# Performance work log

Measured on AMD Instinct MI355X. Metric: run time of the kernel, lower is better.

Reference implementation:

```python
import jax, jax.numpy as jnp
import numpy as np

N_NODES = 131072
D = 256            # nfeat_dim
E = 262144         # edges per graph (pos and neg)
IN_DIM = 2 * D     # 512
HID = IN_DIM // 2  # 256


def setup_inputs() -> dict:
    key = jax.random.key(0)
    k0, k1, k2, k3, k4, k5, k6 = jax.random.split(key, 7)
    block_outputs = jax.random.normal(k0, (N_NODES, D), dtype=jnp.float32)
    pos_src = jax.random.randint(k1, (E,), 0, N_NODES)
    pos_dst = jax.random.randint(k2, (E,), 0, N_NODES)
    neg_src = jax.random.randint(k3, (E,), 0, N_NODES)
    neg_dst = jax.random.randint(k4, (E,), 0, N_NODES)
    # LinkPredLayer params (xavier-normal-like init for weights)
    w1_std = float(np.sqrt(2.0 / (IN_DIM + HID)))
    w2_std = float(np.sqrt(2.0 / (HID + 1)))
    W1 = jax.random.normal(k5, (IN_DIM, HID), dtype=jnp.float32) * w1_std
    b1 = jnp.zeros((HID,), dtype=jnp.float32)
    W2 = jax.random.normal(k6, (HID, 1), dtype=jnp.float32) * w2_std
    b2 = jnp.zeros((1,), dtype=jnp.float32)
    return {"block_outputs": block_outputs, "pos_src": pos_src, "pos_dst": pos_dst,
            "neg_src": neg_src, "neg_dst": neg_dst,
            "W1": W1, "b1": b1, "W2": W2, "b2": b2}


def _linkpred_mlp(h, W1, b1, W2, b2):
    # eval mode: dropout = identity; BatchNorm defined in __init__ but unused in forward
    h = jax.nn.relu(h @ W1 + b1)        # [E_total, HID]
    return jax.nn.sigmoid(h @ W2 + b2)  # [E_total, 1]


def reference(block_outputs, pos_src, pos_dst, neg_src, neg_dst, W1, b1, W2, b2):
    # edge gather: src || dst concat per edge (apply_edges(linkpred_concat))
    pos_emb = jnp.concatenate([block_outputs[pos_src], block_outputs[pos_dst]], axis=1)  # [E, 2D]
    neg_emb = jnp.concatenate([block_outputs[neg_src], block_outputs[neg_dst]], axis=1)  # [E, 2D]
    emb = jnp.concatenate([pos_emb, neg_emb], axis=0)  # [2E, 2D]
    logits = _linkpred_mlp(emb, W1, b1, W2, b2)        # [2E, 1]
    labels = jnp.zeros_like(logits).at[:pos_emb.shape[0]].set(1.0)
    return logits.squeeze(-1), labels.squeeze(-1)
```

## Files before the change

### kernel.cpp

```cpp
#include <hip/hip_runtime.h>
#include <hip/hip_bf16.h>
#include <stdint.h>

#define E_EDGES 262144
#define DFEAT 256
#define KDIM 512
#define NNODES 131072

typedef __attribute__((ext_vector_type(8))) short short8;
typedef __attribute__((ext_vector_type(4))) float f32x4;

static __device__ __forceinline__ unsigned f2bf(float x) {
    unsigned u = __float_as_uint(x);
    u += 0x7fffu + ((u >> 16) & 1u);
    return u >> 16;
}
static __device__ __forceinline__ float bf2f(unsigned short s) {
    return __uint_as_float(((unsigned)s) << 16);
}

__global__ __launch_bounds__(256) void prep_wB2_kernel(const float* __restrict__ W1,
                                                       unsigned short* __restrict__ wB2) {
    int idx = blockIdx.x * 256 + threadIdx.x;
    int n = idx >> 8;
    int k = idx & 255;
    int srow = k + ((n >= 256) ? 256 : 0);
    wB2[((size_t)(k >> 3) * 512 + n) * 8 + (k & 7)] = (unsigned short)f2bf(W1[srow * 256 + (n & 255)]);
}

__global__ __launch_bounds__(512, 2) void gemm_uv5_kernel(const float* __restrict__ table,
                                                          const unsigned short* __restrict__ wB2,
                                                          unsigned short* __restrict__ uv) {
    __shared__ __align__(16) unsigned char lds[65536];

    const int tid = threadIdx.x;
    const int l = tid & 63;
    const int wv = tid >> 6;
    const int l15 = l & 15;
    const int lq = l >> 4;

    short8 bfr[8][4];
#pragma unroll
    for (int kk = 0; kk < 8; ++kk)
#pragma unroll
        for (int j = 0; j < 4; ++j) {
            int col = wv * 64 + j * 16 + l15;
            bfr[kk][j] = *(const short8*)(wB2 + ((size_t)(kk * 4 + lq) * 512 + col) * 8);
        }

    const int srow = tid >> 4;
    const int gc0 = (tid & 15) * 2;
    const int tile0 = blockIdx.x * 16;

    float4 sreg[4];
    auto loadA = [&](int t) {
        const float* src = table + (size_t)(tile0 + t) * 32 * DFEAT + (size_t)srow * DFEAT;
#pragma unroll
        for (int m = 0; m < 2; ++m) {
            sreg[m * 2]     = *(const float4*)(src + (gc0 + m) * 8);
            sreg[m * 2 + 1] = *(const float4*)(src + (gc0 + m) * 8 + 4);
        }
    };
    auto writeA = [&](int buf) {
        unsigned char* base = lds + buf * 16384 + srow * 512;
#pragma unroll
        for (int m = 0; m < 2; ++m) {
            int gc = gc0 + m;
            uint4 w;
            w.x = f2bf(sreg[m * 2].x)     | (f2bf(sreg[m * 2].y) << 16);
            w.y = f2bf(sreg[m * 2].z)     | (f2bf(sreg[m * 2].w) << 16);
            w.z = f2bf(sreg[m * 2 + 1].x) | (f2bf(sreg[m * 2 + 1].y) << 16);
            w.w = f2bf(sreg[m * 2 + 1].z) | (f2bf(sreg[m * 2 + 1].w) << 16);
            int phys = (gc & 16) | ((gc ^ (srow & 15)) & 15);
            *(uint4*)(base + phys * 16) = w;
        }
    };

    loadA(0);
    writeA(0);
    asm volatile("s_waitcnt lgkmcnt(0)" ::: "memory");
    __builtin_amdgcn_s_barrier();

    for (int t = 0; t < 16; ++t) {
        const int m0 = (tile0 + t) * 32;

        if (t < 15) loadA(t + 1);

        f32x4 acc[2][4];
#pragma unroll
        for (int i = 0; i < 2; ++i)
#pragma unroll
            for (int j = 0; j < 4; ++j)
                acc[i][j] = (f32x4){0.f, 0.f, 0.f, 0.f};

        const unsigned char* Ab = lds + (t & 1) * 16384;
#pragma unroll
        for (int kk = 0; kk < 8; ++kk) {
            int g = kk * 4 + lq;
            int phys = (g & 16) | ((g ^ l15) & 15);
            short8 af[2];
#pragma unroll
            for (int i = 0; i < 2; ++i)
                af[i] = *(const short8*)(Ab + (i * 16 + l15) * 512 + phys * 16);
#pragma unroll
            for (int i = 0; i < 2; ++i)
#pragma unroll
                for (int j = 0; j < 4; ++j)
                    acc[i][j] = __builtin_amdgcn_mfma_f32_16x16x32_bf16(bfr[kk][j], af[i], acc[i][j], 0, 0, 0);
        }

        unsigned char* Bnc = lds + 32768;
#pragma unroll
        for (int i = 0; i < 2; ++i)
#pragma unroll
            for (int j = 0; j < 4; ++j) {
                unsigned lo = f2bf(acc[i][j][0]) | (f2bf(acc[i][j][1]) << 16);
                unsigned hi = f2bf(acc[i][j][2]) | (f2bf(acc[i][j][3]) << 16);
                int nodep = i * 16 + l15;
                int colbyte = wv * 128 + j * 32 + lq * 8;
                int g = colbyte >> 4;
                int phys = (g & ~15) | ((g ^ nodep) & 15);
                *(uint2*)(Bnc + nodep * 1024 + phys * 16 + (colbyte & 15)) = make_uint2(lo, hi);
            }

        asm volatile("s_waitcnt lgkmcnt(0)" ::: "memory");
        __builtin_amdgcn_s_barrier();

#pragma unroll
        for (int p = 0; p < 4; ++p) {
            int node = p * 8 + (tid >> 6);
            int col16 = tid & 63;
            int phys = (col16 & ~15) | ((col16 ^ node) & 15);
            uint4 w = *(const uint4*)(Bnc + node * 1024 + phys * 16);
            *(uint4*)(uv + ((size_t)(m0 + node)) * 512 + col16 * 8) = w;
        }

        if (t < 15) writeA((t + 1) & 1);

        asm volatile("s_waitcnt lgkmcnt(0)" ::: "memory");
        __builtin_amdgcn_s_barrier();
    }
}

__global__ __launch_bounds__(256) void edge2_kernel(
    const unsigned short* __restrict__ uv,
    const int* __restrict__ pos_src, const int* __restrict__ pos_dst,
    const int* __restrict__ neg_src, const int* __restrict__ neg_dst,
    const float* __restrict__ b1, const float* __restrict__ W2,
    const float* __restrict__ b2,
    float* __restrict__ out) {

    const int tid = threadIdx.x;
    const int m = tid & 31;
    const int hw = tid >> 5;
    const int eb = blockIdx.x * 64;
    const int e0 = eb + hw * 8;
    const bool is_pos = (eb < E_EDGES);
    const int ee0 = is_pos ? e0 : e0 - E_EDGES;
    const int* __restrict__ srcp = is_pos ? pos_src : neg_src;
    const int* __restrict__ dstp = is_pos ? pos_dst : neg_dst;

    int4 sa = *(const int4*)(srcp + ee0);
    int4 sb = *(const int4*)(srcp + ee0 + 4);
    int4 da = *(const int4*)(dstp + ee0);
    int4 db = *(const int4*)(dstp + ee0 + 4);
    const int sidx[8] = {sa.x, sa.y, sa.z, sa.w, sb.x, sb.y, sb.z, sb.w};
    const int didx[8] = {da.x, da.y, da.z, da.w, db.x, db.y, db.z, db.w};

    short8 uvec[8], vvec[8];
#pragma unroll
    for (int j = 0; j < 8; ++j) {
        uvec[j] = *(const short8*)(uv + (size_t)sidx[j] * 512 + m * 8);
        vvec[j] = *(const short8*)(uv + (size_t)didx[j] * 512 + 256 + m * 8);
    }

    float b1a[8], w2a[8];
    *(float4*)&b1a[0] = *(const float4*)(b1 + m * 8);
    *(float4*)&b1a[4] = *(const float4*)(b1 + m * 8 + 4);
    *(float4*)&w2a[0] = *(const float4*)(W2 + m * 8);
    *(float4*)&w2a[4] = *(const float4*)(W2 + m * 8 + 4);
    const float b2v = b2[0];

    float p[8];
#pragma unroll
    for (int j = 0; j < 8; ++j) {
        float pp = 0.f;
#pragma unroll
        for (int i = 0; i < 8; ++i) {
            float z = bf2f((unsigned short)uvec[j][i]) + bf2f((unsigned short)vvec[j][i]) + b1a[i];
            z = fmaxf(z, 0.f);
            pp = fmaf(z, w2a[i], pp);
        }
#pragma unroll
        for (int mk = 1; mk < 32; mk <<= 1) pp += __shfl_xor(pp, mk, 64);
        p[j] = pp;
    }

    float pj = p[0];
#pragma unroll
    for (int k = 1; k < 8; ++k) if (m == k) pj = p[k];
    if (m < 8) {
        float x = pj + b2v;
        out[(size_t)e0 + m] = 1.0f / (1.0f + __expf(-x));
    }
    if (tid < 64)
        out[(size_t)(2 * E_EDGES) + eb + tid] = is_pos ? 1.0f : 0.0f;
}

__global__ __launch_bounds__(256) void conv_table_kernel(const float* __restrict__ t,
                                                         unsigned short* __restrict__ o) {
    int idx = blockIdx.x * 256 + threadIdx.x;
    float4 a = ((const float4*)t)[idx * 2];
    float4 b = ((const float4*)t)[idx * 2 + 1];
    uint4 w;
    w.x = f2bf(a.x) | (f2bf(a.y) << 16);
    w.y = f2bf(a.z) | (f2bf(a.w) << 16);
    w.z = f2bf(b.x) | (f2bf(b.y) << 16);
    w.w = f2bf(b.z) | (f2bf(b.w) << 16);
    ((uint4*)o)[idx] = w;
}

__global__ __launch_bounds__(256) void prep_w1t_kernel(const float* __restrict__ W1,
                                                       unsigned short* __restrict__ w1t) {
    int idx = blockIdx.x * 256 + threadIdx.x;
    int k = idx >> 8;
    int n = idx & 255;
    w1t[n * KDIM + k] = (unsigned short)f2bf(W1[idx]);
}

__global__ __launch_bounds__(256) void linkpred4_kernel(
    const unsigned short* __restrict__ tblb,
    const int* __restrict__ pos_src, const int* __restrict__ pos_dst,
    const int* __restrict__ neg_src, const int* __restrict__ neg_dst,
    const float* __restrict__ b1, const float* __restrict__ W2,
    const float* __restrict__ b2,
    const unsigned short* __restrict__ w1t,
    float* __restrict__ out) {

    __shared__ __align__(16) unsigned short Bs[64 * 512];

    const int tid = threadIdx.x;
    const int l = tid & 63;
    const int wv = tid >> 6;
    const int l15 = l & 15;
    const int lq = l >> 4;
    const int m0 = blockIdx.x * 128;
    const bool is_pos = (m0 < E_EDGES);

    int nsrc[2], ndst[2];
#pragma unroll
    for (int mt = 0; mt < 2; ++mt) {
        int m = m0 + wv * 32 + mt * 16 + l15;
        if (is_pos) { nsrc[mt] = pos_src[m];            ndst[mt] = pos_dst[m]; }
        else        { int mm = m - E_EDGES; nsrc[mt] = neg_src[mm]; ndst[mt] = neg_dst[mm]; }
    }

    auto stageB = [&](int c) {
#pragma unroll
        for (int i = 0; i < 16; ++i) {
            int lc = wv * 16 + i;
            int gc = c * 64 + lc;
            const unsigned short* g = w1t + (size_t)gc * KDIM + ((l ^ i) << 3);
            char* lp = (char*)Bs + lc * 1024;
            __builtin_amdgcn_global_load_lds(
                (const __attribute__((address_space(1))) void*)g,
                (__attribute__((address_space(3))) void*)lp, 16, 0, 0);
        }
    };

    stageB(0);
    __builtin_amdgcn_sched_barrier(0);

    short8 af[2][16];
#pragma unroll
    for (int h = 0; h < 16; ++h)
#pragma unroll
        for (int mt = 0; mt < 2; ++mt) {
            int node = (h < 8) ? nsrc[mt] : ndst[mt];
            const unsigned short* g = tblb + (size_t)node * DFEAT + (h & 7) * 32 + lq * 8;
            af[mt][h] = *(const short8*)g;
        }
    __builtin_amdgcn_sched_barrier(0);

    f32x4 acc[2][4];
#pragma unroll
    for (int mt = 0; mt < 2; ++mt)
#pragma unroll
        for (int j = 0; j < 4; ++j)
            acc[mt][j] = (f32x4){0.f, 0.f, 0.f, 0.f};
    float rowacc[2][4] = {{0.f, 0.f, 0.f, 0.f}, {0.f, 0.f, 0.f, 0.f}};

    const char* Bb = (const char*)Bs;

#pragma unroll
    for (int c = 0; c < 4; ++c) {
        if (c == 0) {
            asm volatile("s_waitcnt vmcnt(32)" ::: "memory");
        } else {
            __syncthreads();
            stageB(c);
#pragma unroll
            for (int mt = 0; mt < 2; ++mt)
#pragma unroll
                for (int j = 0; j < 4; ++j) {
                    int col = (c - 1) * 64 + j * 16 + l15;
                    float b1v = b1[col], w2v = W2[col];
#pragma unroll
                    for (int r = 0; r < 4; ++r) {
                        float hv = fmaxf(acc[mt][j][r] + b1v, 0.f);
                        rowacc[mt][r] = fmaf(hv, w2v, rowacc[mt][r]);
                    }
                    acc[mt][j] = (f32x4){0.f, 0.f, 0.f, 0.f};
                }
            asm volatile("s_waitcnt vmcnt(0)" ::: "memory");
        }
        __builtin_amdgcn_s_barrier();

        __builtin_amdgcn_s_setprio(1);
#pragma unroll
        for (int h = 0; h < 16; ++h) {
            short8 bf[4];
#pragma unroll
            for (int j = 0; j < 4; ++j) {
                int cl = j * 16 + l15;
                int phys = (h * 4 + lq) ^ l15;
                bf[j] = *(const short8*)(Bb + cl * 1024 + phys * 16);
            }
#pragma unroll
            for (int mt = 0; mt < 2; ++mt)
#pragma unroll
                for (int j = 0; j < 4; ++j)
                    acc[mt][j] = __builtin_amdgcn_mfma_f32_16x16x32_bf16(af[mt][h], bf[j], acc[mt][j], 0, 0, 0);
        }
        __builtin_amdgcn_s_setprio(0);
    }

#pragma unroll
    for (int mt = 0; mt < 2; ++mt)
#pragma unroll
        for (int j = 0; j < 4; ++j) {
            int col = 3 * 64 + j * 16 + l15;
            float b1v = b1[col], w2v = W2[col];
#pragma unroll
            for (int r = 0; r < 4; ++r) {
                float hv = fmaxf(acc[mt][j][r] + b1v, 0.f);
                rowacc[mt][r] = fmaf(hv, w2v, rowacc[mt][r]);
            }
        }

    const float b2v = b2[0];
#pragma unroll
    for (int mt = 0; mt < 2; ++mt)
#pragma unroll
        for (int r = 0; r < 4; ++r) {
            float p = rowacc[mt][r];
#pragma unroll
            for (int mk = 1; mk < 16; mk <<= 1) p += __shfl_xor(p, mk, 64);
            if (l15 == 0) {
                int m = m0 + wv * 32 + mt * 16 + lq * 4 + r;
                float sg = 1.0f / (1.0f + __expf(-(p + b2v)));
                out[(size_t)m] = sg;
                out[(size_t)(2 * E_EDGES) + m] = is_pos ? 1.0f : 0.0f;
            }
        }
}

__global__ __launch_bounds__(256) void linkpred_fb_kernel(
    const float* __restrict__ table,
    const int* __restrict__ pos_src, const int* __restrict__ pos_dst,
    const int* __restrict__ neg_src, const int* __restrict__ neg_dst,
    const float* __restrict__ b1, const float* __restrict__ W2,
    const float* __restrict__ b2,
    const unsigned short* __restrict__ w1t,
    float* __restrict__ out) {

    __shared__ __align__(16) unsigned short As[2][64 * 64];
    __shared__ int sIdx[64], dIdx[64];
    __shared__ float wpart[4][64];

    const int tid = threadIdx.x;
    const int l = tid & 63;
    const int wv = tid >> 6;
    const int m0 = blockIdx.x * 64;

    if (tid < 64) {
        int m = m0 + tid;
        int si, di;
        if (m < E_EDGES) { si = pos_src[m];            di = pos_dst[m]; }
        else             { si = neg_src[m - E_EDGES];  di = neg_dst[m - E_EDGES]; }
        sIdx[tid] = si;
        dIdx[tid] = di;
    }

    float b1v[4], w2v[4];
#pragma unroll
    for (int j = 0; j < 4; j++) {
        int n = wv * 64 + j * 16 + (l & 15);
        b1v[j] = b1[n];
        w2v[j] = W2[n];
    }

    __syncthreads();

    const int e0 = tid >> 3;
    const int q  = tid & 7;
    const int e1 = e0 + 32;

    auto pack_write = [&](int buf, int e, const float4& x, const float4& y) {
        uint4 w;
        w.x = f2bf(x.x) | (f2bf(x.y) << 16);
        w.y = f2bf(x.z) | (f2bf(x.w) << 16);
        w.z = f2bf(y.x) | (f2bf(y.y) << 16);
        w.w = f2bf(y.z) | (f2bf(y.w) << 16);
        int byte = e * 128 + q * 16;
        byte ^= (e & 7) << 4;
        *(uint4*)((char*)(&As[buf][0]) + byte) = w;
    };

    {
        const float* p0 = table + (size_t)sIdx[e0] * DFEAT + q * 8;
        const float* p1 = table + (size_t)sIdx[e1] * DFEAT + q * 8;
        float4 a0 = *(const float4*)p0, a1 = *(const float4*)(p0 + 4);
        float4 c0 = *(const float4*)p1, c1 = *(const float4*)(p1 + 4);
        pack_write(0, e0, a0, a1);
        pack_write(0, e1, c0, c1);
    }
    __syncthreads();

    f32x4 acc[4][4];
#pragma unroll
    for (int i = 0; i < 4; i++)
#pragma unroll
        for (int j = 0; j < 4; j++)
            acc[i][j] = (f32x4){0.f, 0.f, 0.f, 0.f};

    for (int s = 0; s < 8; s++) {
        float4 a0, a1, c0, c1;
        if (s < 7) {
            int sn = s + 1;
            const int* idxA = (sn < 4) ? sIdx : dIdx;
            int cb = (sn & 3) * 64 + q * 8;
            const float* p0 = table + (size_t)idxA[e0] * DFEAT + cb;
            const float* p1 = table + (size_t)idxA[e1] * DFEAT + cb;
            a0 = *(const float4*)p0; a1 = *(const float4*)(p0 + 4);
            c0 = *(const float4*)p1; c1 = *(const float4*)(p1 + 4);
        }

        const int cur = s & 1;
        const char* Abase = (const char*)(&As[cur][0]);
#pragma unroll
        for (int h = 0; h < 2; h++) {
            short8 af[4], bf[4];
#pragma unroll
            for (int i = 0; i < 4; i++) {
                int row = i * 16 + (l & 15);
                int byte = row * 128 + h * 64 + ((l >> 4) << 4);
                byte ^= (l & 7) << 4;
                af[i] = *(const short8*)(Abase + byte);
            }
#pragma unroll
            for (int j = 0; j < 4; j++) {
                int col = wv * 64 + j * 16 + (l & 15);
                int koff = s * 64 + h * 32 + ((l >> 4) << 3);
                bf[j] = *(const short8*)(w1t + col * KDIM + koff);
            }
#pragma unroll
            for (int i = 0; i < 4; i++)
#pragma unroll
                for (int j = 0; j < 4; j++)
                    acc[i][j] = __builtin_amdgcn_mfma_f32_16x16x32_bf16(af[i], bf[j], acc[i][j], 0, 0, 0);
        }

        if (s < 7) {
            pack_write((s + 1) & 1, e0, a0, a1);
            pack_write((s + 1) & 1, e1, c0, c1);
        }
        __syncthreads();
    }

    float part[16];
#pragma unroll
    for (int i = 0; i < 4; i++) {
#pragma unroll
        for (int r = 0; r < 4; r++) {
            float p = 0.f;
#pragma unroll
            for (int j = 0; j < 4; j++) {
                float hv = acc[i][j][r] + b1v[j];
                hv = fmaxf(hv, 0.f);
                p = fmaf(hv, w2v[j], p);
            }
#pragma unroll
            for (int mk = 1; mk < 16; mk <<= 1) p += __shfl_xor(p, mk, 64);
            part[i * 4 + r] = p;
        }
    }
    if ((l & 15) == 0) {
        int g = l >> 4;
#pragma unroll
        for (int i = 0; i < 4; i++)
#pragma unroll
            for (int r = 0; r < 4; r++)
                wpart[wv][i * 16 + g * 4 + r] = part[i * 4 + r];
    }
    __syncthreads();

    if (tid < 64) {
        float x = wpart[0][tid] + wpart[1][tid] + wpart[2][tid] + wpart[3][tid] + b2[0];
        float sg = 1.0f / (1.0f + __expf(-x));
        out[(size_t)m0 + tid] = sg;
        out[(size_t)(2 * E_EDGES) + m0 + tid] = (m0 < E_EDGES) ? 1.0f : 0.0f;
    }
}

extern "C" void kernel_launch(void* const* d_in, const int* in_sizes, int n_in,
                              void* d_out, int out_size, void* d_ws, size_t ws_size,
                              hipStream_t stream) {
    const float* table = (const float*)d_in[0];
    const int* ps = (const int*)d_in[1];
    const int* pd = (const int*)d_in[2];
    const int* ns = (const int*)d_in[3];
    const int* nd = (const int*)d_in[4];
    const float* W1 = (const float*)d_in[5];
    const float* b1 = (const float*)d_in[6];
    const float* W2 = (const float*)d_in[7];
    const float* b2 = (const float*)d_in[8];
    float* out = (float*)d_out;

    const size_t wB_bytes  = (size_t)KDIM * 256 * 2;
    const size_t uv_bytes  = (size_t)NNODES * KDIM * 2;
    const size_t tbl_bytes = (size_t)NNODES * DFEAT * 2;
    const size_t w1t_bytes = (size_t)256 * KDIM * 2;

    if (ws_size >= wB_bytes + uv_bytes) {
        unsigned short* wB2 = (unsigned short*)d_ws;
        unsigned short* uv = (unsigned short*)((char*)d_ws + wB_bytes);
        hipLaunchKernelGGL(prep_wB2_kernel, dim3(512), dim3(256), 0, stream, W1, wB2);
        hipLaunchKernelGGL(gemm_uv5_kernel, dim3(256), dim3(512), 0, stream, table, wB2, uv);
        hipLaunchKernelGGL(edge2_kernel, dim3(8192), dim3(256), 0, stream,
                           uv, ps, pd, ns, nd, b1, W2, b2, out);
    } else if (ws_size >= tbl_bytes + w1t_bytes) {
        unsigned short* tblb = (unsigned short*)d_ws;
        unsigned short* w1t = (unsigned short*)((char*)d_ws + tbl_bytes);
        hipLaunchKernelGGL(conv_table_kernel, dim3(16384), dim3(256), 0, stream, table, tblb);
        hipLaunchKernelGGL(prep_w1t_kernel, dim3(512), dim3(256), 0, stream, W1, w1t);
        hipLaunchKernelGGL(linkpred4_kernel, dim3(4096), dim3(256), 0, stream,
                           tblb, ps, pd, ns, nd, b1, W2, b2, w1t, out);
    } else {
        unsigned short* w1t = (unsigned short*)d_ws;
        hipLaunchKernelGGL(prep_w1t_kernel, dim3(512), dim3(256), 0, stream, W1, w1t);
        hipLaunchKernelGGL(linkpred_fb_kernel, dim3(8192), dim3(256), 0, stream,
                           table, ps, pd, ns, nd, b1, W2, b2, w1t, out);
    }
}
```

Before: 141.6 us.

## Deepen GEMM prefetch to two tiles and defer uv stores to next tile

The node-projection GEMM now holds two register buffers, so global loads for tile t+2 are issued while tile t computes, instead of only one tile ahead. The global store of each tile's bf16 result is moved into the start of the next iteration, after the barrier, so it overlaps with the next tile's MFMA work rather than sitting between barriers. The loop is manually unrolled by two through macros so the register buffers alternate. This raises register pressure and could reduce occupancy or cause spills under the (512,2) launch bounds.

```diff
diff --git a/kernel.cpp b/kernel.cpp
--- a/kernel.cpp
+++ b/kernel.cpp
@@ -28,7 +28,7 @@
     wB2[((size_t)(k >> 3) * 512 + n) * 8 + (k & 7)] = (unsigned short)f2bf(W1[srow * 256 + (n & 255)]);
 }
 
-__global__ __launch_bounds__(512, 2) void gemm_uv5_kernel(const float* __restrict__ table,
+__global__ __launch_bounds__(512, 2) void gemm_uv6_kernel(const float* __restrict__ table,
                                                           const unsigned short* __restrict__ wB2,
                                                           unsigned short* __restrict__ uv) {
     __shared__ __align__(16) unsigned char lds[65536];
@@ -52,94 +52,112 @@
     const int gc0 = (tid & 15) * 2;
     const int tile0 = blockIdx.x * 16;
 
-    float4 sreg[4];
-    auto loadA = [&](int t) {
-        const float* src = table + (size_t)(tile0 + t) * 32 * DFEAT + (size_t)srow * DFEAT;
-#pragma unroll
-        for (int m = 0; m < 2; ++m) {
-            sreg[m * 2]     = *(const float4*)(src + (gc0 + m) * 8);
-            sreg[m * 2 + 1] = *(const float4*)(src + (gc0 + m) * 8 + 4);
-        }
-    };
-    auto writeA = [&](int buf) {
-        unsigned char* base = lds + buf * 16384 + srow * 512;
-#pragma unroll
-        for (int m = 0; m < 2; ++m) {
-            int gc = gc0 + m;
-            uint4 w;
-            w.x = f2bf(sreg[m * 2].x)     | (f2bf(sreg[m * 2].y) << 16);
-            w.y = f2bf(sreg[m * 2].z)     | (f2bf(sreg[m * 2].w) << 16);
-            w.z = f2bf(sreg[m * 2 + 1].x) | (f2bf(sreg[m * 2 + 1].y) << 16);
-            w.w = f2bf(sreg[m * 2 + 1].z) | (f2bf(sreg[m * 2 + 1].w) << 16);
-            int phys = (gc & 16) | ((gc ^ (srow & 15)) & 15);
-            *(uint4*)(base + phys * 16) = w;
-        }
-    };
-
-    loadA(0);
-    writeA(0);
+    float4 sregA[4], sregB[4];
+
+#define LOADTO(T, S)                                                               \
+    {                                                                              \
+        const float* _src = table + (size_t)(tile0 + (T)) * 32 * DFEAT             \
+                            + (size_t)srow * DFEAT;                                \
+        _Pragma("unroll")                                                          \
+        for (int _m = 0; _m < 2; ++_m) {                                           \
+            S[_m * 2]     = *(const float4*)(_src + (gc0 + _m) * 8);               \
+            S[_m * 2 + 1] = *(const float4*)(_src + (gc0 + _m) * 8 + 4);           \
+        }                                                                          \
+    }
+
+#define WRITEA(BUF, S)                                                             \
+    {                                                                              \
+        unsigned char* _base = lds + (BUF) * 16384 + srow * 512;                   \
+        _Pragma("unroll")                                                          \
+        for (int _m = 0; _m < 2; ++_m) {                                           \
+            int _gc = gc0 + _m;                                                    \
+            uint4 _w;                                                              \
+            _w.x = f2bf(S[_m * 2].x)     | (f2bf(S[_m * 2].y) << 16);              \
+            _w.y = f2bf(S[_m * 2].z)     | (f2bf(S[_m * 2].w) << 16);              \
+            _w.z = f2bf(S[_m * 2 + 1].x) | (f2bf(S[_m * 2 + 1].y) << 16);          \
+            _w.w = f2bf(S[_m * 2 + 1].z) | (f2bf(S[_m * 2 + 1].w) << 16);          \
+            int _phys = (_gc & 16) | ((_gc ^ (srow & 15)) & 15);                   \
+            *(uint4*)(_base + _phys * 16) = _w;                                    \
+        }                                                                          \
+    }
+
+#define STORE_PREV(T)                                                              \
+    {                                                                              \
+        const int _m0 = (tile0 + (T)-1) * 32;                                      \
+        unsigned char* _bnc = lds + 32768;                                         \
+        _Pragma("unroll")                                                          \
+        for (int _p = 0; _p < 4; ++_p) {                                           \
+            int _node = _p * 8 + wv;                                               \
+            int _c16 = l;                                                          \
+            int _phys = (_c16 & ~15) | ((_c16 ^ _node) & 15);                      \
+            uint4 _w = *(const uint4*)(_bnc + _node * 1024 + _phys * 16);          \
+            *(uint4*)(uv + ((size_t)(_m0 + _node)) * 512 + _c16 * 8) = _w;         \
+        }                                                                          \
+    }
+
+#define TILE_BODY(T, LDST, WSRC, ABUF)                                             \
+    {                                                                              \
+        if ((T) > 0) STORE_PREV(T);                                                \
+        if ((T) + 2 < 16) LOADTO((T) + 2, LDST);                                   \
+        f32x4 acc[2][4];                                                           \
+        _Pragma("unroll")                                                          \
+        for (int _i = 0; _i < 2; ++_i)                                             \
+            _Pragma("unroll")                                                      \
+            for (int _j = 0; _j < 4; ++_j)                                         \
+                acc[_i][_j] = (f32x4){0.f, 0.f, 0.f, 0.f};                         \
+        const unsigned char* _Ab = lds + (ABUF) * 16384;                           \
+        _Pragma("unroll")                                                          \
+        for (int _kk = 0; _kk < 8; ++_kk) {                                        \
+            int _g = _kk * 4 + lq;                                                 \
+            int _phys = (_g & 16) | ((_g ^ l15) & 15);                             \
+            short8 _af[2];                                                         \
+            _Pragma("unroll")                                                      \
+            for (int _i = 0; _i < 2; ++_i)                                         \
+                _af[_i] = *(const short8*)(_Ab + (_i * 16 + l15) * 512 + _phys * 16); \
+            _Pragma("unroll")                                                      \
+            for (int _i = 0; _i < 2; ++_i)                                         \
+                _Pragma("unroll")                                                  \
+                for (int _j = 0; _j < 4; ++_j)                                     \
+                    acc[_i][_j] = __builtin_amdgcn_mfma_f32_16x16x32_bf16(         \
+                        bfr[_kk][_j], _af[_i], acc[_i][_j], 0, 0, 0);              \
+        }                                                                          \
+        asm volatile("s_waitcnt lgkmcnt(0)" ::: "memory");                         \
+        __builtin_amdgcn_s_barrier();                                              \
+        unsigned char* _bnc = lds + 32768;                                         \
+        _Pragma("unroll")                                                          \
+        for (int _i = 0; _i < 2; ++_i)                                             \
+            _Pragma("unroll")                                                      \
+            for (int _j = 0; _j < 4; ++_j) {                                       \
+                unsigned _lo = f2bf(acc[_i][_j][0]) | (f2bf(acc[_i][_j][1]) << 16);\
+                unsigned _hi = f2bf(acc[_i][_j][2]) | (f2bf(acc[_i][_j][3]) << 16);\
+                int _nodep = _i * 16 + l15;                                        \
+                int _cb = wv * 128 + _j * 32 + lq * 8;                             \
+                int _g = _cb >> 4;                                                 \
+                int _phys = (_g & ~15) | ((_g ^ _nodep) & 15);                     \
+                *(uint2*)(_bnc + _nodep * 1024 + _phys * 16 + (_cb & 15)) =        \
+                    make_uint2(_lo, _hi);                                          \
+            }                                                                      \
+        if ((T) < 15) WRITEA(((T) + 1) & 1, WSRC);                                 \
+        asm volatile("s_waitcnt lgkmcnt(0)" ::: "memory");                         \
+        __builtin_amdgcn_s_barrier();                                              \
+    }
+
+    LOADTO(0, sregA);
+    WRITEA(0, sregA);
+    LOADTO(1, sregB);
     asm volatile("s_waitcnt lgkmcnt(0)" ::: "memory");
     __builtin_amdgcn_s_barrier();
 
-    for (int t = 0; t < 16; ++t) {
-        const int m0 = (tile0 + t) * 32;
-
-        if (t < 15) loadA(t + 1);
-
-        f32x4 acc[2][4];
-#pragma unroll
-        for (int i = 0; i < 2; ++i)
-#pragma unroll
-            for (int j = 0; j < 4; ++j)
-                acc[i][j] = (f32x4){0.f, 0.f, 0.f, 0.f};
-
-        const unsigned char* Ab = lds + (t & 1) * 16384;
-#pragma unroll
-        for (int kk = 0; kk < 8; ++kk) {
-            int g = kk * 4 + lq;
-            int phys = (g & 16) | ((g ^ l15) & 15);
-            short8 af[2];
-#pragma unroll
-            for (int i = 0; i < 2; ++i)
-                af[i] = *(const short8*)(Ab + (i * 16 + l15) * 512 + phys * 16);
-#pragma unroll
-            for (int i = 0; i < 2; ++i)
-#pragma unroll
-                for (int j = 0; j < 4; ++j)
-                    acc[i][j] = __builtin_amdgcn_mfma_f32_16x16x32_bf16(bfr[kk][j], af[i], acc[i][j], 0, 0, 0);
-        }
-
-        unsigned char* Bnc = lds + 32768;
-#pragma unroll
-        for (int i = 0; i < 2; ++i)
-#pragma unroll
-            for (int j = 0; j < 4; ++j) {
-                unsigned lo = f2bf(acc[i][j][0]) | (f2bf(acc[i][j][1]) << 16);
-                unsigned hi = f2bf(acc[i][j][2]) | (f2bf(acc[i][j][3]) << 16);
-                int nodep = i * 16 + l15;
-                int colbyte = wv * 128 + j * 32 + lq * 8;
-                int g = colbyte >> 4;
-                int phys = (g & ~15) | ((g ^ nodep) & 15);
-                *(uint2*)(Bnc + nodep * 1024 + phys * 16 + (colbyte & 15)) = make_uint2(lo, hi);
-            }
-
-        asm volatile("s_waitcnt lgkmcnt(0)" ::: "memory");
-        __builtin_amdgcn_s_barrier();
-
-#pragma unroll
-        for (int p = 0; p < 4; ++p) {
-            int node = p * 8 + (tid >> 6);
-            int col16 = tid & 63;
-            int phys = (col16 & ~15) | ((col16 ^ node) & 15);
-            uint4 w = *(const uint4*)(Bnc + node * 1024 + phys * 16);
-            *(uint4*)(uv + ((size_t)(m0 + node)) * 512 + col16 * 8) = w;
-        }
-
-        if (t < 15) writeA((t + 1) & 1);
-
-        asm volatile("s_waitcnt lgkmcnt(0)" ::: "memory");
-        __builtin_amdgcn_s_barrier();
-    }
+    for (int tt = 0; tt < 16; tt += 2) {
+        TILE_BODY(tt, sregA, sregB, 0);
+        TILE_BODY(tt + 1, sregB, sregA, 1);
+    }
+    STORE_PREV(16);
+
+#undef TILE_BODY
+#undef STORE_PREV
+#undef WRITEA
+#undef LOADTO
 }
 
 __global__ __launch_bounds__(256) void edge2_kernel(
@@ -536,7 +554,7 @@
         unsigned short* wB2 = (unsigned short*)d_ws;
         unsigned short* uv = (unsigned short*)((char*)d_ws + wB_bytes);
         hipLaunchKernelGGL(prep_wB2_kernel, dim3(512), dim3(256), 0, stream, W1, wB2);
-        hipLaunchKernelGGL(gemm_uv5_kernel, dim3(256), dim3(512), 0, stream, table, wB2, uv);
+        hipLaunchKernelGGL(gemm_uv6_kernel, dim3(256), dim3(512), 0, stream, table, wB2, uv);
         hipLaunchKernelGGL(edge2_kernel, dim3(8192), dim3(256), 0, stream,
                            uv, ps, pd, ns, nd, b1, W2, b2, out);
     } else if (ws_size >= tbl_bytes + w1t_bytes) {
```

Result: no change. 140.9 us (-0.5%).
